# Optimization experiments

Hardware: AMD Instinct MI355X
Metric: run time of the kernel (lower is better)

## Reference

```python
import jax, jax.numpy as jnp
import numpy as np

BN_EPS = 1e-4  # matches torch.nn.BatchNorm1d(eps=0.0001)

def setup_inputs() -> dict:
    key = jax.random.key(0)
    ks = jax.random.split(key, 8)
    N, T, D_in, D_out = 512, 64, 1024, 1024
    return {
        "input_feature_st": jax.random.randint(ks[0], (N, T, D_in), 0, 2).astype(jnp.float32),
        "input_features_sc": jax.random.normal(ks[1], (N, D_in), dtype=jnp.float32),
        "weight": jax.random.normal(ks[2], (D_out, D_in), dtype=jnp.float32) * 0.03,
        "bias": jax.random.normal(ks[3], (D_out,), dtype=jnp.float32) * 0.1,
        "gamma": jax.random.normal(ks[4], (D_out,), dtype=jnp.float32) * 2.0,  # nn.init.normal_(bn.weight, 0, 2.0)
        "beta": jnp.zeros((D_out,), dtype=jnp.float32),
        "running_mean": jax.random.normal(ks[5], (D_out,), dtype=jnp.float32) * 0.1,
        "running_var": jax.random.uniform(ks[6], (D_out,), dtype=jnp.float32, minval=0.5, maxval=1.5),
    }

def _if_scan(pot_in, bias_step):
    # pot_in: (N, T, D_out); bias_step: (D_out,) -> spikes (N, T, D_out)
    pot0 = jnp.zeros(pot_in.shape[::2], dtype=pot_in.dtype)  # (N, D_out)
    def step(pot, p_t):
        pot = pot + p_t + bias_step
        spk = (pot >= 1.0).astype(pot.dtype)
        return pot - spk, spk
    _, spikes_t = jax.lax.scan(step, pot0, jnp.swapaxes(pot_in, 0, 1))  # (T, N, D)
    return jnp.swapaxes(spikes_t, 0, 1)

def reference(input_feature_st, input_features_sc, weight, bias, gamma, beta, running_mean, running_var):
    T = input_feature_st.shape[1]
    # ANN path: Linear + BN (eval stats) + ReLU
    lin = input_features_sc @ weight.T + bias                      # (N, D_out)
    out_bn = gamma * (lin - running_mean) / jnp.sqrt(running_var + BN_EPS) + beta
    ann_output = jax.nn.relu(out_bn)
    # Fold BN into weights for the SNN path (note: no eps, as in source)
    ratio = gamma / jnp.sqrt(running_var)
    w_norm = weight * ratio[:, None]                               # (D_out, D_in)
    b_norm = (bias - running_mean) * ratio + beta                  # (D_out,)
    # Integrate-and-fire scan over T
    pot_in = jnp.einsum("ntd,od->nto", input_feature_st, w_norm)  # (N, T, D_out)
    spike_out = _if_scan(pot_in, b_norm / T)
    spike_count_out = jnp.sum(spike_out, axis=1)                   # (N, D_out)
    return spike_out, spike_count_out
```

## Files before the change

### kernel.cpp

```cpp
#include <hip/hip_runtime.h>
#include <hip/hip_bf16.h>

typedef float  float4v __attribute__((ext_vector_type(4)));
typedef short  short8v __attribute__((ext_vector_type(8)));
typedef short  short4v __attribute__((ext_vector_type(4)));
typedef __bf16 bf16x8  __attribute__((ext_vector_type(8)));
typedef float  f32x4   __attribute__((ext_vector_type(4)));

constexpr int NB = 512, T = 64, DIN = 1024, DOUT = 1024;

constexpr size_t ABF_BYTES = (size_t)NB * T * DIN * 2;
constexpr size_t WN_BYTES  = (size_t)DOUT * DIN * 2;
constexpr size_t WS_BF16   = ABF_BYTES + WN_BYTES;

__device__ __forceinline__ short f2bf_rne(float x) {
    return __builtin_bit_cast(short, __float2bfloat16(x));
}
__device__ __forceinline__ short f2bf_trunc(float x) {
    return (short)(__builtin_bit_cast(unsigned int, x) >> 16);
}
__device__ __forceinline__ void load_lds_16B(const void* g, void* l) {
    __builtin_amdgcn_global_load_lds(
        (const __attribute__((address_space(1))) unsigned int*)g,
        (__attribute__((address_space(3))) unsigned int*)l, 16, 0, 0);
}

constexpr int PREP_A_BLOCKS = NB * T * DIN / 8 / 256;
constexpr int PREP_W_BLOCKS = DOUT * DIN / 4 / 256;

__global__ void __launch_bounds__(256)
prep_fused(const float* __restrict__ A, short* __restrict__ Abf,
           const float* __restrict__ W, const float* __restrict__ gamma,
           const float* __restrict__ rvar, short* __restrict__ Wn) {
    const int b = blockIdx.x;
    if (b < PREP_A_BLOCKS) {
        int idx = b * 256 + threadIdx.x;
        const float4v* p = (const float4v*)A + (size_t)idx * 2;
        float4v v0 = __builtin_nontemporal_load(p);
        float4v v1 = __builtin_nontemporal_load(p + 1);
        short8v s;
        #pragma unroll
        for (int j = 0; j < 4; j++) {
            s[j]     = f2bf_trunc(v0[j]);
            s[j + 4] = f2bf_trunc(v1[j]);
        }
        *((short8v*)Abf + idx) = s;
    } else {
        int idx = (b - PREP_A_BLOCKS) * 256 + threadIdx.x;
        int o = idx >> 8;
        float r = gamma[o] / sqrtf(rvar[o]);
        float4v w = ((const float4v*)W)[idx];
        short4v s;
        #pragma unroll
        for (int j = 0; j < 4; j++) s[j] = f2bf_rne(w[j] * r);
        ((short4v*)Wn)[idx] = s;
    }
}

__global__ void __launch_bounds__(256)
fold_w_kernel(const float* __restrict__ W, const float* __restrict__ gamma,
              const float* __restrict__ rvar, short* __restrict__ Wn) {
    int idx = blockIdx.x * 256 + threadIdx.x;
    int o = idx >> 8;
    float r = gamma[o] / sqrtf(rvar[o]);
    float4v w = ((const float4v*)W)[idx];
    short4v s;
    #pragma unroll
    for (int j = 0; j < 4; j++) s[j] = f2bf_rne(w[j] * r);
    ((short4v*)Wn)[idx] = s;
}

constexpr int BM2 = 256, BN2 = 256, BK2 = 32;
constexpr int NSTEP2 = DIN / BK2;
constexpr int BUFB   = (BM2 + BN2) * BK2 * 2;
constexpr int BREG   = BM2 * BK2 * 2;

__global__ void __launch_bounds__(512, 2)
snn_gemm_if_256(const short* __restrict__ Abf,
                const short* __restrict__ Wn,
                const float* __restrict__ bias, const float* __restrict__ gamma,
                const float* __restrict__ beta, const float* __restrict__ rmean,
                const float* __restrict__ rvar, float* __restrict__ out) {
    __shared__ __align__(16) char sm[3 * BUFB];
    __shared__ float bstepS[BN2];

    const int tid = threadIdx.x;
    const int oB  = blockIdx.x * BN2;
    const int bs  = blockIdx.y;

    if (tid < BN2) {
        int o = oB + tid;
        float r = gamma[o] / sqrtf(rvar[o]);
        bstepS[tid] = ((bias[o] - rmean[o]) * r + beta[o]) * (1.0f / 64.0f);
    }

    const int lane = tid & 63;
    const int wv   = tid >> 6;
    const int wr   = wv >> 2;
    const int wc   = wv & 3;
    const int l15  = lane & 15;
    const int quad = lane >> 4;

    int aOff[8], bOff[4];
    #pragma unroll
    for (int mi = 0; mi < 8; mi++) {
        int r = wr * 128 + mi * 16 + l15;
        aOff[mi] = (r * 4 + (quad ^ ((r >> 1) & 3))) * 16;
    }
    #pragma unroll
    for (int ni = 0; ni < 4; ni++) {
        int r = wc * 64 + ni * 16 + l15;
        bOff[ni] = BREG + (r * 4 + (quad ^ ((r >> 1) & 3))) * 16;
    }

    f32x4 acc[8][4] = {};

    const int s0 = tid, s1 = 512 + tid;
    const int r0 = s0 >> 2, r1 = s1 >> 2;
    const int c0 = (s0 & 3) ^ ((r0 >> 1) & 3);
    const int c1 = (s1 & 3) ^ ((r1 >> 1) & 3);
    const short* gA0 = Abf + (size_t)(bs * BM2 + r0) * DIN + c0 * 8;
    const short* gA1 = Abf + (size_t)(bs * BM2 + r1) * DIN + c1 * 8;
    const short* gB0 = Wn + (size_t)(oB + r0) * DIN + c0 * 8;
    const short* gB1 = Wn + (size_t)(oB + r1) * DIN + c1 * 8;
    const int dA0 = s0 * 16, dA1 = s1 * 16;
    const int dB0 = BREG + s0 * 16, dB1 = BREG + s1 * 16;

    auto STAGE = [&](int bufB) {
        load_lds_16B(gA0, sm + bufB + dA0);
        load_lds_16B(gA1, sm + bufB + dA1);
        load_lds_16B(gB0, sm + bufB + dB0);
        load_lds_16B(gB1, sm + bufB + dB1);
        gA0 += BK2; gA1 += BK2; gB0 += BK2; gB1 += BK2;
    };
    auto COMPUTE = [&](int bufB) {
        const char* base = sm + bufB;
        bf16x8 af[8], bv[4];
        #pragma unroll
        for (int mi = 0; mi < 8; mi++)
            af[mi] = __builtin_bit_cast(bf16x8, *(const short8v*)(base + aOff[mi]));
        #pragma unroll
        for (int ni = 0; ni < 4; ni++)
            bv[ni] = __builtin_bit_cast(bf16x8, *(const short8v*)(base + bOff[ni]));
        __builtin_amdgcn_s_setprio(1);
        #pragma unroll
        for (int mi = 0; mi < 8; mi++)
            #pragma unroll
            for (int ni = 0; ni < 4; ni++)
                acc[mi][ni] = __builtin_amdgcn_mfma_f32_16x16x32_bf16(
                    af[mi], bv[ni], acc[mi][ni], 0, 0, 0);
        __builtin_amdgcn_s_setprio(0);
    };

    STAGE(0);
    STAGE(BUFB);
    asm volatile("s_waitcnt vmcnt(4)" ::: "memory");
    __builtin_amdgcn_sched_barrier(0);
    __builtin_amdgcn_s_barrier();
    __builtin_amdgcn_sched_barrier(0);

    int cb = 0, sb = 2 * BUFB;
    #pragma unroll 1
    for (int t = 0; t < NSTEP2 - 2; ++t) {
        STAGE(sb);
        COMPUTE(cb);
        asm volatile("s_waitcnt vmcnt(4)" ::: "memory");
        __builtin_amdgcn_sched_barrier(0);
        __builtin_amdgcn_s_barrier();
        __builtin_amdgcn_sched_barrier(0);
        cb = (cb == 2 * BUFB) ? 0 : cb + BUFB;
        sb = (sb == 2 * BUFB) ? 0 : sb + BUFB;
    }
    COMPUTE(0);
    asm volatile("s_waitcnt vmcnt(0)" ::: "memory");
    __builtin_amdgcn_sched_barrier(0);
    __builtin_amdgcn_s_barrier();
    __builtin_amdgcn_sched_barrier(0);
    COMPUTE(BUFB);

    __syncthreads();

    float* potS = (float*)sm;
    #pragma unroll
    for (int s = 0; s < 4; ++s) {
        if (wr == (s >> 1)) {
            const int mib = (s & 1) * 4;
            #pragma unroll
            for (int m2 = 0; m2 < 4; ++m2)
                #pragma unroll
                for (int ni = 0; ni < 4; ++ni)
                    #pragma unroll
                    for (int r = 0; r < 4; ++r) {
                        int rl  = m2 * 16 + quad * 4 + r;
                        int col = (wc * 64 + ni * 16 + l15) ^ (quad << 3);
                        potS[rl * BN2 + col] = acc[mib + m2][ni][r];
                    }
        }
        __syncthreads();
        if (tid < BN2) {
            int n = bs * 4 + s;
            float pot = 0.f, cnt = 0.f;
            const float bst = bstepS[tid];
            float* so = out + (size_t)n * T * DOUT + oB + tid;
            for (int t = 0; t < T; t++) {
                pot += potS[t * BN2 + (tid ^ (((t >> 2) & 3) << 3))] + bst;
                float spk = (pot >= 1.0f) ? 1.0f : 0.0f;
                pot -= spk;
                cnt += spk;
                __builtin_nontemporal_store(spk, so + (size_t)t * DOUT);
            }
            __builtin_nontemporal_store(
                cnt, out + (size_t)NB * T * DOUT + (size_t)n * DOUT + oB + tid);
        }
        __syncthreads();
    }
}


constexpr int BM = 128, BN = 128, BK = 64;
constexpr int LDA_F = 72;
constexpr int A_BYTES_F = BM * LDA_F * 2;
constexpr int SMEM_F = A_BYTES_F + BN * BK * 2;

template <bool PREFOLD>
__global__ void __launch_bounds__(256)
snn_gemm_if(const float* __restrict__ A, const float* __restrict__ W,
            const short* __restrict__ Wn,
            const float* __restrict__ bias, const float* __restrict__ gamma,
            const float* __restrict__ beta, const float* __restrict__ rmean,
            const float* __restrict__ rvar, float* __restrict__ out) {
    __shared__ __align__(16) char smem[SMEM_F];
    __shared__ float ratioS[BN];
    __shared__ float bstepS[BN];
    short* AsS  = (short*)smem;
    short* BsS  = (short*)(smem + A_BYTES_F);
    float* potS = (float*)smem;

    const int tid   = threadIdx.x;
    const int by    = blockIdx.y;
    const int oBase = blockIdx.x * BN;

    if (tid < BN) {
        int o = oBase + tid;
        float r = gamma[o] / sqrtf(rvar[o]);
        ratioS[tid] = r;
        bstepS[tid] = ((bias[o] - rmean[o]) * r + beta[o]) * (1.0f / 64.0f);
    }
    __syncthreads();

    const int lane = tid & 63;
    const int wv   = tid >> 6;
    const int wr   = wv & 1;
    const int wc   = wv >> 1;
    const int l15  = lane & 15;
    const int quad = lane >> 4;

    f32x4 acc[4][4] = {};
    const float* Ab = A + (size_t)by * BM * DIN;

    for (int kb = 0; kb < DIN; kb += BK) {
        float4v av[4][2];
        #pragma unroll
        for (int i = 0; i < 4; i++) {
            int g = i * 256 + tid;
            int r = g >> 3, k8 = g & 7;
            const float4v* p = (const float4v*)(Ab + (size_t)r * DIN + kb + k8 * 8);
            av[i][0] = p[0];
            av[i][1] = p[1];
        }
        float4v bv[4][2];
        if constexpr (!PREFOLD) {
            #pragma unroll
            for (int i = 0; i < 4; i++) {
                int slot = i * 256 + tid;
                int r = slot >> 3, k8 = (slot & 7) ^ (r & 7);
                const float4v* p = (const float4v*)(W + (size_t)(oBase + r) * DIN + kb + k8 * 8);
                bv[i][0] = p[0];
                bv[i][1] = p[1];
            }
        }
        __syncthreads();

        if constexpr (PREFOLD) {
            #pragma unroll
            for (int i = 0; i < 4; i++) {
                int slot = i * 256 + tid;
                int r = slot >> 3, k8 = (slot & 7) ^ (r & 7);
                load_lds_16B(Wn + (size_t)(oBase + r) * DIN + kb + k8 * 8,
                             BsS + (size_t)slot * 8);
            }
        } else {
            #pragma unroll
            for (int i = 0; i < 4; i++) {
                int slot = i * 256 + tid;
                int r = slot >> 3;
                float rt = ratioS[r];
                short8v s;
                #pragma unroll
                for (int j = 0; j < 4; j++) {
                    s[j]     = f2bf_rne(bv[i][0][j] * rt);
                    s[j + 4] = f2bf_rne(bv[i][1][j] * rt);
                }
                *(short8v*)(BsS + (size_t)slot * 8) = s;
            }
        }
        #pragma unroll
        for (int i = 0; i < 4; i++) {
            int g = i * 256 + tid;
            int r = g >> 3, k8 = g & 7;
            short8v s;
            #pragma unroll
            for (int j = 0; j < 4; j++) {
                s[j]     = f2bf_trunc(av[i][0][j]);
                s[j + 4] = f2bf_trunc(av[i][1][j]);
            }
            *(short8v*)(&AsS[r * LDA_F + k8 * 8]) = s;
        }
        __syncthreads();

        #pragma unroll
        for (int ks = 0; ks < 2; ks++) {
            bf16x8 af[4], bfv[4];
            #pragma unroll
            for (int mi = 0; mi < 4; mi++)
                af[mi] = __builtin_bit_cast(bf16x8,
                    *(const short8v*)(&AsS[(wr * 64 + mi * 16 + l15) * LDA_F + ks * 32 + quad * 8]));
            #pragma unroll
            for (int ni = 0; ni < 4; ni++) {
                int row  = wc * 64 + ni * 16 + l15;
                int slot = row * 8 + ((ks * 4 + quad) ^ (l15 & 7));
                bfv[ni] = __builtin_bit_cast(bf16x8, *(const short8v*)(BsS + (size_t)slot * 8));
            }
            #pragma unroll
            for (int mi = 0; mi < 4; mi++)
                #pragma unroll
                for (int ni = 0; ni < 4; ni++)
                    acc[mi][ni] = __builtin_amdgcn_mfma_f32_16x16x32_bf16(
                        af[mi], bfv[ni], acc[mi][ni], 0, 0, 0);
        }
    }

    __syncthreads();

    #pragma unroll 1
    for (int s = 0; s < 2; s++) {
        if (wr == s) {
            #pragma unroll
            for (int mi = 0; mi < 4; mi++)
                #pragma unroll
                for (int ni = 0; ni < 4; ni++)
                    #pragma unroll
                    for (int r = 0; r < 4; r++)
                        potS[(mi * 16 + quad * 4 + r) * BN + wc * 64 + ni * 16 + l15] =
                            acc[mi][ni][r];
        }
        __syncthreads();
        if (tid < BN) {
            int n = by * 2 + s;
            float pot = 0.f, cnt = 0.f;
            const float bst = bstepS[tid];
            float* so = out + (size_t)n * T * DOUT + oBase + tid;
            for (int t = 0; t < T; t++) {
                pot += potS[t * BN + tid] + bst;
                float spk = (pot >= 1.0f) ? 1.0f : 0.0f;
                pot -= spk;
                cnt += spk;
                so[(size_t)t * DOUT] = spk;
            }
            out[(size_t)NB * T * DOUT + (size_t)n * DOUT + oBase + tid] = cnt;
        }
        __syncthreads();
    }
}

extern "C" void kernel_launch(void* const* d_in, const int* in_sizes, int n_in,
                              void* d_out, int out_size, void* d_ws, size_t ws_size,
                              hipStream_t stream) {
    const float* A     = (const float*)d_in[0];
    const float* W     = (const float*)d_in[2];
    const float* bias  = (const float*)d_in[3];
    const float* gamma = (const float*)d_in[4];
    const float* beta  = (const float*)d_in[5];
    const float* rmean = (const float*)d_in[6];
    const float* rvar  = (const float*)d_in[7];
    float* out = (float*)d_out;

    if (d_ws != nullptr && ws_size >= WS_BF16) {
        short* Abf = (short*)d_ws;
        short* Wn  = (short*)((char*)d_ws + ABF_BYTES);
        prep_fused<<<PREP_A_BLOCKS + PREP_W_BLOCKS, 256, 0, stream>>>(
            A, Abf, W, gamma, rvar, Wn);
        dim3 grid(DOUT / BN2, NB / 4);
        snn_gemm_if_256<<<grid, 512, 0, stream>>>(Abf, Wn, bias, gamma, beta,
                                                  rmean, rvar, out);
    } else if (d_ws != nullptr && ws_size >= WN_BYTES) {
        short* Wn = (short*)d_ws;
        fold_w_kernel<<<DOUT * DIN / 4 / 256, 256, 0, stream>>>(W, gamma, rvar, Wn);
        dim3 grid(DOUT / BN, NB / 2);
        snn_gemm_if<true><<<grid, 256, 0, stream>>>(A, W, Wn, bias, gamma, beta,
                                                    rmean, rvar, out);
    } else {
        dim3 grid(DOUT / BN, NB / 2);
        snn_gemm_if<false><<<grid, 256, 0, stream>>>(A, W, nullptr, bias, gamma, beta,
                                                     rmean, rvar, out);
    }
}
```

Baseline: 320.7 us.

## Restructure 256x256 SNN GEMM into 9-slot LDS ring with interleaved quarter-tile MFMA phases

The bf16 GEMM main loop now uses BK=64 and a 9-slot LDS ring in 16KB half-tile slots. Loads for future A/B halves are issued between four MFMA phases, each bracketed by barriers, so global-to-LDS traffic overlaps compute at a finer grain. The grid becomes 1D with an XCD-aware remap of block index to work tile for better L2 locality. The IF scan epilogue now uses all 512 threads, two samples at a time, instead of 256. LDS use rises to about 144KB, which could limit occupancy to one block per CU despite the launch bound of 2, and the extra barriers add sync cost.

After: 321.4 us. About the same (+0.2%).

```diff
diff --git a/kernel.cpp b/kernel.cpp
--- a/kernel.cpp
+++ b/kernel.cpp
@@ -70,10 +70,11 @@
     ((short4v*)Wn)[idx] = s;
 }
 
-constexpr int BM2 = 256, BN2 = 256, BK2 = 32;
-constexpr int NSTEP2 = DIN / BK2;
-constexpr int BUFB   = (BM2 + BN2) * BK2 * 2;
-constexpr int BREG   = BM2 * BK2 * 2;
+constexpr int BM2 = 256, BN2 = 256, BK2 = 64;
+constexpr int NT2   = DIN / BK2;
+constexpr int SLOT  = 16384;
+constexpr int NSLOT = 9;
+constexpr int RINGB = NSLOT * SLOT;
 
 __global__ void __launch_bounds__(512, 2)
 snn_gemm_if_256(const short* __restrict__ Abf,
@@ -81,18 +82,21 @@
                 const float* __restrict__ bias, const float* __restrict__ gamma,
                 const float* __restrict__ beta, const float* __restrict__ rmean,
                 const float* __restrict__ rvar, float* __restrict__ out) {
-    __shared__ __align__(16) char sm[3 * BUFB];
+    __shared__ __align__(16) char sm[RINGB];
     __shared__ float bstepS[BN2];
 
     const int tid = threadIdx.x;
-    const int oB  = blockIdx.x * BN2;
-    const int bs  = blockIdx.y;
+    const int work = (blockIdx.x & 7) * 64 + (blockIdx.x >> 3);
+    const int oB = (work & 3) * BN2;
+    const int rg = work >> 2;
 
     if (tid < BN2) {
         int o = oB + tid;
         float r = gamma[o] / sqrtf(rvar[o]);
         bstepS[tid] = ((bias[o] - rmean[o]) * r + beta[o]) * (1.0f / 64.0f);
     }
+    asm volatile("s_waitcnt vmcnt(0)" ::: "memory");
+    __builtin_amdgcn_sched_barrier(0);
 
     const int lane = tid & 63;
     const int wv   = tid >> 6;
@@ -101,116 +105,172 @@
     const int l15  = lane & 15;
     const int quad = lane >> 4;
 
-    int aOff[8], bOff[4];
-    #pragma unroll
-    for (int mi = 0; mi < 8; mi++) {
-        int r = wr * 128 + mi * 16 + l15;
-        aOff[mi] = (r * 4 + (quad ^ ((r >> 1) & 3))) * 16;
-    }
-    #pragma unroll
-    for (int ni = 0; ni < 4; ni++) {
-        int r = wc * 64 + ni * 16 + l15;
-        bOff[ni] = BREG + (r * 4 + (quad ^ ((r >> 1) & 3))) * 16;
-    }
+    const int D0 = l15 * 128 + ((quad ^ (l15 & 7)) * 16);
+    const int D1 = l15 * 128 + (((4 + quad) ^ (l15 & 7)) * 16);
+    const int bWoff = (wc & 1) * 8192;
+
+    const int row0 = tid >> 3,         ck0 = (tid & 7) ^ (row0 & 7);
+    const int row1 = (512 + tid) >> 3, ck1 = ((512 + tid) & 7) ^ (row1 & 7);
+    const short* gA0a = Abf + (size_t)(rg * BM2 + row0) * DIN + ck0 * 8;
+    const short* gA0b = Abf + (size_t)(rg * BM2 + row1) * DIN + ck1 * 8;
+    const short* gA1a = gA0a + (size_t)128 * DIN;
+    const short* gA1b = gA0b + (size_t)128 * DIN;
+    const short* gB0a = Wn + (size_t)(oB + row0) * DIN + ck0 * 8;
+    const short* gB0b = Wn + (size_t)(oB + row1) * DIN + ck1 * 8;
+    const short* gB1a = gB0a + (size_t)128 * DIN;
+    const short* gB1b = gB0b + (size_t)128 * DIN;
+
+    auto STAGE = [&](const short*& g0, const short*& g1, int dstB) {
+        load_lds_16B(g0, sm + dstB + tid * 16);
+        load_lds_16B(g1, sm + dstB + 8192 + tid * 16);
+        g0 += BK2; g1 += BK2;
+    };
+    auto LD8 = [&](const char* p) {
+        return __builtin_bit_cast(bf16x8, *(const short8v*)p);
+    };
 
     f32x4 acc[8][4] = {};
 
-    const int s0 = tid, s1 = 512 + tid;
-    const int r0 = s0 >> 2, r1 = s1 >> 2;
-    const int c0 = (s0 & 3) ^ ((r0 >> 1) & 3);
-    const int c1 = (s1 & 3) ^ ((r1 >> 1) & 3);
-    const short* gA0 = Abf + (size_t)(bs * BM2 + r0) * DIN + c0 * 8;
-    const short* gA1 = Abf + (size_t)(bs * BM2 + r1) * DIN + c1 * 8;
-    const short* gB0 = Wn + (size_t)(oB + r0) * DIN + c0 * 8;
-    const short* gB1 = Wn + (size_t)(oB + r1) * DIN + c1 * 8;
-    const int dA0 = s0 * 16, dA1 = s1 * 16;
-    const int dB0 = BREG + s0 * 16, dB1 = BREG + s1 * 16;
-
-    auto STAGE = [&](int bufB) {
-        load_lds_16B(gA0, sm + bufB + dA0);
-        load_lds_16B(gA1, sm + bufB + dA1);
-        load_lds_16B(gB0, sm + bufB + dB0);
-        load_lds_16B(gB1, sm + bufB + dB1);
-        gA0 += BK2; gA1 += BK2; gB0 += BK2; gB1 += BK2;
-    };
-    auto COMPUTE = [&](int bufB) {
-        const char* base = sm + bufB;
-        bf16x8 af[8], bv[4];
-        #pragma unroll
-        for (int mi = 0; mi < 8; mi++)
-            af[mi] = __builtin_bit_cast(bf16x8, *(const short8v*)(base + aOff[mi]));
-        #pragma unroll
-        for (int ni = 0; ni < 4; ni++)
-            bv[ni] = __builtin_bit_cast(bf16x8, *(const short8v*)(base + bOff[ni]));
-        __builtin_amdgcn_s_setprio(1);
-        #pragma unroll
-        for (int mi = 0; mi < 8; mi++)
-            #pragma unroll
-            for (int ni = 0; ni < 4; ni++)
-                acc[mi][ni] = __builtin_amdgcn_mfma_f32_16x16x32_bf16(
-                    af[mi], bv[ni], acc[mi][ni], 0, 0, 0);
-        __builtin_amdgcn_s_setprio(0);
-    };
-
-    STAGE(0);
-    STAGE(BUFB);
-    asm volatile("s_waitcnt vmcnt(4)" ::: "memory");
+    int rbA0 = 0, rbA1 = SLOT, rbB0 = 2 * SLOT, rbB1 = 3 * SLOT;
+    int wb0 = 5 * SLOT, wb1 = 6 * SLOT, wb2 = 7 * SLOT, wb3 = 8 * SLOT;
+    auto adv = [](int& x) { x += 4 * SLOT; if (x >= RINGB) x -= RINGB; };
+
+    STAGE(gA0a, gA0b, 0);
+    STAGE(gA1a, gA1b, SLOT);
+    STAGE(gB0a, gB0b, 2 * SLOT);
+    STAGE(gB1a, gB1b, 3 * SLOT);
+    STAGE(gA0a, gA0b, 4 * SLOT);
+    asm volatile("s_waitcnt vmcnt(2)" ::: "memory");
     __builtin_amdgcn_sched_barrier(0);
     __builtin_amdgcn_s_barrier();
     __builtin_amdgcn_sched_barrier(0);
 
-    int cb = 0, sb = 2 * BUFB;
     #pragma unroll 1
-    for (int t = 0; t < NSTEP2 - 2; ++t) {
-        STAGE(sb);
-        COMPUTE(cb);
-        asm volatile("s_waitcnt vmcnt(4)" ::: "memory");
+    for (int t = 0; t < NT2; ++t) {
+        const char* pA = sm + (wr ? rbA1 : rbA0);
+        const char* pB = sm + ((wc & 2) ? rbB1 : rbB0) + bWoff;
+        bf16x8 af[4][2], bfv[2][2], bf2[2][2];
+
+        if (t < NT2 - 1) { STAGE(gA1a, gA1b, wb0); STAGE(gB0a, gB0b, wb1); }
+        #pragma unroll
+        for (int mi = 0; mi < 4; mi++) {
+            af[mi][0] = LD8(pA + mi * 2048 + D0);
+            af[mi][1] = LD8(pA + mi * 2048 + D1);
+        }
+        #pragma unroll
+        for (int ni = 0; ni < 2; ni++) {
+            bfv[ni][0] = LD8(pB + ni * 2048 + D0);
+            bfv[ni][1] = LD8(pB + ni * 2048 + D1);
+        }
+        __builtin_amdgcn_s_barrier();
+        __builtin_amdgcn_s_setprio(1);
+        #pragma unroll
+        for (int mi = 0; mi < 4; mi++)
+            #pragma unroll
+            for (int ni = 0; ni < 2; ni++)
+                #pragma unroll
+                for (int ks = 0; ks < 2; ks++)
+                    acc[mi][ni] = __builtin_amdgcn_mfma_f32_16x16x32_bf16(
+                        af[mi][ks], bfv[ni][ks], acc[mi][ni], 0, 0, 0);
+        __builtin_amdgcn_s_setprio(0);
+        __builtin_amdgcn_s_barrier();
+
+        if (t < NT2 - 1) STAGE(gB1a, gB1b, wb2);
+        if (t < NT2 - 2) STAGE(gA0a, gA0b, wb3);
+        #pragma unroll
+        for (int ni = 0; ni < 2; ni++) {
+            bf2[ni][0] = LD8(pB + (2 + ni) * 2048 + D0);
+            bf2[ni][1] = LD8(pB + (2 + ni) * 2048 + D1);
+        }
+        __builtin_amdgcn_s_barrier();
+        __builtin_amdgcn_s_setprio(1);
+        #pragma unroll
+        for (int mi = 0; mi < 4; mi++)
+            #pragma unroll
+            for (int ni = 0; ni < 2; ni++)
+                #pragma unroll
+                for (int ks = 0; ks < 2; ks++)
+                    acc[mi][2 + ni] = __builtin_amdgcn_mfma_f32_16x16x32_bf16(
+                        af[mi][ks], bf2[ni][ks], acc[mi][2 + ni], 0, 0, 0);
+        __builtin_amdgcn_s_setprio(0);
+        __builtin_amdgcn_s_barrier();
+
+        #pragma unroll
+        for (int mi = 0; mi < 4; mi++) {
+            af[mi][0] = LD8(pA + (4 + mi) * 2048 + D0);
+            af[mi][1] = LD8(pA + (4 + mi) * 2048 + D1);
+        }
+        __builtin_amdgcn_s_barrier();
+        __builtin_amdgcn_s_setprio(1);
+        #pragma unroll
+        for (int mi = 0; mi < 4; mi++)
+            #pragma unroll
+            for (int ni = 0; ni < 2; ni++)
+                #pragma unroll
+                for (int ks = 0; ks < 2; ks++)
+                    acc[4 + mi][ni] = __builtin_amdgcn_mfma_f32_16x16x32_bf16(
+                        af[mi][ks], bfv[ni][ks], acc[4 + mi][ni], 0, 0, 0);
+        __builtin_amdgcn_s_setprio(0);
+        __builtin_amdgcn_s_barrier();
+
+        __builtin_amdgcn_s_setprio(1);
+        #pragma unroll
+        for (int mi = 0; mi < 4; mi++)
+            #pragma unroll
+            for (int ni = 0; ni < 2; ni++)
+                #pragma unroll
+                for (int ks = 0; ks < 2; ks++)
+                    acc[4 + mi][2 + ni] = __builtin_amdgcn_mfma_f32_16x16x32_bf16(
+                        af[mi][ks], bf2[ni][ks], acc[4 + mi][2 + ni], 0, 0, 0);
+        __builtin_amdgcn_s_setprio(0);
+
+        if (t == NT2 - 2) {
+            asm volatile("s_waitcnt vmcnt(0)" ::: "memory");
+        } else {
+            asm volatile("s_waitcnt vmcnt(2)" ::: "memory");
+        }
         __builtin_amdgcn_sched_barrier(0);
         __builtin_amdgcn_s_barrier();
         __builtin_amdgcn_sched_barrier(0);
-        cb = (cb == 2 * BUFB) ? 0 : cb + BUFB;
-        sb = (sb == 2 * BUFB) ? 0 : sb + BUFB;
-    }
-    COMPUTE(0);
-    asm volatile("s_waitcnt vmcnt(0)" ::: "memory");
-    __builtin_amdgcn_sched_barrier(0);
-    __builtin_amdgcn_s_barrier();
-    __builtin_amdgcn_sched_barrier(0);
-    COMPUTE(BUFB);
+
+        adv(rbA0); adv(rbA1); adv(rbB0); adv(rbB1);
+        adv(wb0);  adv(wb1);  adv(wb2);  adv(wb3);
+    }
 
     __syncthreads();
 
     float* potS = (float*)sm;
-    #pragma unroll
-    for (int s = 0; s < 4; ++s) {
-        if (wr == (s >> 1)) {
-            const int mib = (s & 1) * 4;
-            #pragma unroll
-            for (int m2 = 0; m2 < 4; ++m2)
-                #pragma unroll
-                for (int ni = 0; ni < 4; ++ni)
+    #pragma unroll 1
+    for (int rd = 0; rd < 2; ++rd) {
+        if (wr == rd) {
+            #pragma unroll
+            for (int mi = 0; mi < 8; mi++)
+                #pragma unroll
+                for (int ni = 0; ni < 4; ni++)
                     #pragma unroll
-                    for (int r = 0; r < 4; ++r) {
-                        int rl  = m2 * 16 + quad * 4 + r;
-                        int col = (wc * 64 + ni * 16 + l15) ^ (quad << 3);
-                        potS[rl * BN2 + col] = acc[mib + m2][ni][r];
+                    for (int r = 0; r < 4; r++) {
+                        int rowl = mi * 16 + quad * 4 + r;
+                        int col  = (wc * 64 + ni * 16 + l15) ^ (quad << 3);
+                        potS[rowl * BN2 + col] = acc[mi][ni][r];
                     }
         }
         __syncthreads();
-        if (tid < BN2) {
-            int n = bs * 4 + s;
+        {
+            int sl = tid >> 8;
+            int c  = tid & 255;
+            int n  = rg * 4 + rd * 2 + sl;
             float pot = 0.f, cnt = 0.f;
-            const float bst = bstepS[tid];
-            float* so = out + (size_t)n * T * DOUT + oB + tid;
-            for (int t = 0; t < T; t++) {
-                pot += potS[t * BN2 + (tid ^ (((t >> 2) & 3) << 3))] + bst;
+            const float bst = bstepS[c];
+            float* so = out + (size_t)n * T * DOUT + oB + c;
+            for (int tt = 0; tt < T; tt++) {
+                pot += potS[(sl * 64 + tt) * BN2 + (c ^ (((tt >> 2) & 3) << 3))] + bst;
                 float spk = (pot >= 1.0f) ? 1.0f : 0.0f;
                 pot -= spk;
                 cnt += spk;
-                __builtin_nontemporal_store(spk, so + (size_t)t * DOUT);
+                __builtin_nontemporal_store(spk, so + (size_t)tt * DOUT);
             }
             __builtin_nontemporal_store(
-                cnt, out + (size_t)NB * T * DOUT + (size_t)n * DOUT + oB + tid);
+                cnt, out + (size_t)NB * T * DOUT + (size_t)n * DOUT + oB + c);
         }
         __syncthreads();
     }
@@ -390,9 +450,8 @@
         short* Wn  = (short*)((char*)d_ws + ABF_BYTES);
         prep_fused<<<PREP_A_BLOCKS + PREP_W_BLOCKS, 256, 0, stream>>>(
             A, Abf, W, gamma, rvar, Wn);
-        dim3 grid(DOUT / BN2, NB / 4);
-        snn_gemm_if_256<<<grid, 512, 0, stream>>>(Abf, Wn, bias, gamma, beta,
-                                                  rmean, rvar, out);
+        snn_gemm_if_256<<<dim3(512), 512, 0, stream>>>(Abf, Wn, bias, gamma, beta,
+                                                       rmean, rvar, out);
     } else if (d_ws != nullptr && ws_size >= WN_BYTES) {
         short* Wn = (short*)d_ws;
         fold_w_kernel<<<DOUT * DIN / 4 / 256, 256, 0, stream>>>(W, gamma, rvar, Wn);
```

## Use 1024-thread blocks with smaller per-wave tiles and all-thread IF scan

Applied to the files above, without the earlier changes.

Doubles the block to 1024 threads (16 waves), so each wave now owns a 64x64 accumulator tile instead of 128x64. This cuts register pressure and lets all threads take part in the integrate-and-fire epilogue: four samples are scanned in parallel, in chunks of 16 timesteps. It also flattens the grid into a 1D launch with a swizzled block-to-tile mapping meant to improve L2 reuse. The trade-off is fewer MFMAs per LDS fragment load, which lowers operand reuse per wave, and launch_bounds(1024,4) may be unattainable given the LDS size.

Result: slower. 346.1 us (+7.9%).

```diff
diff --git a/kernel.cpp b/kernel.cpp
--- a/kernel.cpp
+++ b/kernel.cpp
@@ -71,11 +71,11 @@
 }
 
 constexpr int BM2 = 256, BN2 = 256, BK2 = 32;
-constexpr int NSTEP2 = DIN / BK2;
-constexpr int BUFB   = (BM2 + BN2) * BK2 * 2;
-constexpr int BREG   = BM2 * BK2 * 2;
-
-__global__ void __launch_bounds__(512, 2)
+constexpr int NT2  = DIN / BK2;
+constexpr int BUFB = (BM2 + BN2) * BK2 * 2;
+constexpr int BREG = BM2 * BK2 * 2;
+
+__global__ void __launch_bounds__(1024, 4)
 snn_gemm_if_256(const short* __restrict__ Abf,
                 const short* __restrict__ Wn,
                 const float* __restrict__ bias, const float* __restrict__ gamma,
@@ -85,14 +85,17 @@
     __shared__ float bstepS[BN2];
 
     const int tid = threadIdx.x;
-    const int oB  = blockIdx.x * BN2;
-    const int bs  = blockIdx.y;
+    const int work = (blockIdx.x & 7) * 64 + (blockIdx.x >> 3);
+    const int oB = (work & 3) * BN2;
+    const int rg = work >> 2;
 
     if (tid < BN2) {
         int o = oB + tid;
         float r = gamma[o] / sqrtf(rvar[o]);
         bstepS[tid] = ((bias[o] - rmean[o]) * r + beta[o]) * (1.0f / 64.0f);
     }
+    asm volatile("s_waitcnt vmcnt(0)" ::: "memory");
+    __builtin_amdgcn_sched_barrier(0);
 
     const int lane = tid & 63;
     const int wv   = tid >> 6;
@@ -101,119 +104,105 @@
     const int l15  = lane & 15;
     const int quad = lane >> 4;
 
-    int aOff[8], bOff[4];
+    int aOff[4], bOff[4];
     #pragma unroll
-    for (int mi = 0; mi < 8; mi++) {
-        int r = wr * 128 + mi * 16 + l15;
-        aOff[mi] = (r * 4 + (quad ^ ((r >> 1) & 3))) * 16;
-    }
-    #pragma unroll
-    for (int ni = 0; ni < 4; ni++) {
-        int r = wc * 64 + ni * 16 + l15;
-        bOff[ni] = BREG + (r * 4 + (quad ^ ((r >> 1) & 3))) * 16;
-    }
-
-    f32x4 acc[8][4] = {};
-
-    const int s0 = tid, s1 = 512 + tid;
-    const int r0 = s0 >> 2, r1 = s1 >> 2;
-    const int c0 = (s0 & 3) ^ ((r0 >> 1) & 3);
-    const int c1 = (s1 & 3) ^ ((r1 >> 1) & 3);
-    const short* gA0 = Abf + (size_t)(bs * BM2 + r0) * DIN + c0 * 8;
-    const short* gA1 = Abf + (size_t)(bs * BM2 + r1) * DIN + c1 * 8;
-    const short* gB0 = Wn + (size_t)(oB + r0) * DIN + c0 * 8;
-    const short* gB1 = Wn + (size_t)(oB + r1) * DIN + c1 * 8;
-    const int dA0 = s0 * 16, dA1 = s1 * 16;
-    const int dB0 = BREG + s0 * 16, dB1 = BREG + s1 * 16;
+    for (int i = 0; i < 4; i++) {
+        int ra = wr * 64 + i * 16 + l15;
+        int rb = wc * 64 + i * 16 + l15;
+        aOff[i] = ra * 64 + ((quad ^ ((ra >> 1) & 3)) * 16);
+        bOff[i] = BREG + rb * 64 + ((quad ^ ((rb >> 1) & 3)) * 16);
+    }
+
+    const int srow = tid >> 2;
+    const int gck  = (tid & 3) ^ ((srow >> 1) & 3);
+    const short* gA = Abf + (size_t)(rg * BM2 + srow) * DIN + gck * 8;
+    const short* gB = Wn + (size_t)(oB + srow) * DIN + gck * 8;
+    const int dA = tid * 16;
+    const int dB = BREG + tid * 16;
 
     auto STAGE = [&](int bufB) {
-        load_lds_16B(gA0, sm + bufB + dA0);
-        load_lds_16B(gA1, sm + bufB + dA1);
-        load_lds_16B(gB0, sm + bufB + dB0);
-        load_lds_16B(gB1, sm + bufB + dB1);
-        gA0 += BK2; gA1 += BK2; gB0 += BK2; gB1 += BK2;
+        load_lds_16B(gA, sm + bufB + dA);
+        load_lds_16B(gB, sm + bufB + dB);
+        gA += BK2; gB += BK2;
     };
-    auto COMPUTE = [&](int bufB) {
-        const char* base = sm + bufB;
-        bf16x8 af[8], bv[4];
-        #pragma unroll
-        for (int mi = 0; mi < 8; mi++)
-            af[mi] = __builtin_bit_cast(bf16x8, *(const short8v*)(base + aOff[mi]));
-        #pragma unroll
-        for (int ni = 0; ni < 4; ni++)
-            bv[ni] = __builtin_bit_cast(bf16x8, *(const short8v*)(base + bOff[ni]));
+    auto LD8 = [&](const char* p) {
+        return __builtin_bit_cast(bf16x8, *(const short8v*)p);
+    };
+
+    f32x4 acc[4][4] = {};
+
+    STAGE(0);
+    STAGE(BUFB);
+    asm volatile("s_waitcnt vmcnt(2)" ::: "memory");
+    __builtin_amdgcn_sched_barrier(0);
+    __builtin_amdgcn_s_barrier();
+    __builtin_amdgcn_sched_barrier(0);
+
+    int cb = 0, sb = 2 * BUFB;
+    #pragma unroll 1
+    for (int t = 0; t < NT2; ++t) {
+        if (t < NT2 - 2) STAGE(sb);
+        const char* base = sm + cb;
+        bf16x8 af[4], bv[4];
+        #pragma unroll
+        for (int i = 0; i < 4; i++) af[i] = LD8(base + aOff[i]);
+        #pragma unroll
+        for (int i = 0; i < 4; i++) bv[i] = LD8(base + bOff[i]);
         __builtin_amdgcn_s_setprio(1);
         #pragma unroll
-        for (int mi = 0; mi < 8; mi++)
+        for (int mi = 0; mi < 4; mi++)
             #pragma unroll
             for (int ni = 0; ni < 4; ni++)
                 acc[mi][ni] = __builtin_amdgcn_mfma_f32_16x16x32_bf16(
                     af[mi], bv[ni], acc[mi][ni], 0, 0, 0);
         __builtin_amdgcn_s_setprio(0);
-    };
-
-    STAGE(0);
-    STAGE(BUFB);
-    asm volatile("s_waitcnt vmcnt(4)" ::: "memory");
-    __builtin_amdgcn_sched_barrier(0);
-    __builtin_amdgcn_s_barrier();
-    __builtin_amdgcn_sched_barrier(0);
-
-    int cb = 0, sb = 2 * BUFB;
-    #pragma unroll 1
-    for (int t = 0; t < NSTEP2 - 2; ++t) {
-        STAGE(sb);
-        COMPUTE(cb);
-        asm volatile("s_waitcnt vmcnt(4)" ::: "memory");
+
+        if (t < NT2 - 2) {
+            asm volatile("s_waitcnt vmcnt(2)" ::: "memory");
+        } else {
+            asm volatile("s_waitcnt vmcnt(0)" ::: "memory");
+        }
         __builtin_amdgcn_sched_barrier(0);
         __builtin_amdgcn_s_barrier();
         __builtin_amdgcn_sched_barrier(0);
+
         cb = (cb == 2 * BUFB) ? 0 : cb + BUFB;
         sb = (sb == 2 * BUFB) ? 0 : sb + BUFB;
     }
-    COMPUTE(0);
-    asm volatile("s_waitcnt vmcnt(0)" ::: "memory");
-    __builtin_amdgcn_sched_barrier(0);
-    __builtin_amdgcn_s_barrier();
-    __builtin_amdgcn_sched_barrier(0);
-    COMPUTE(BUFB);
-
-    __syncthreads();
 
     float* potS = (float*)sm;
-    #pragma unroll
-    for (int s = 0; s < 4; ++s) {
-        if (wr == (s >> 1)) {
-            const int mib = (s & 1) * 4;
-            #pragma unroll
-            for (int m2 = 0; m2 < 4; ++m2)
-                #pragma unroll
-                for (int ni = 0; ni < 4; ++ni)
-                    #pragma unroll
-                    for (int r = 0; r < 4; ++r) {
-                        int rl  = m2 * 16 + quad * 4 + r;
-                        int col = (wc * 64 + ni * 16 + l15) ^ (quad << 3);
-                        potS[rl * BN2 + col] = acc[mib + m2][ni][r];
-                    }
-        }
-        __syncthreads();
-        if (tid < BN2) {
-            int n = bs * 4 + s;
-            float pot = 0.f, cnt = 0.f;
-            const float bst = bstepS[tid];
-            float* so = out + (size_t)n * T * DOUT + oB + tid;
-            for (int t = 0; t < T; t++) {
-                pot += potS[t * BN2 + (tid ^ (((t >> 2) & 3) << 3))] + bst;
-                float spk = (pot >= 1.0f) ? 1.0f : 0.0f;
-                pot -= spk;
-                cnt += spk;
-                __builtin_nontemporal_store(spk, so + (size_t)t * DOUT);
-            }
-            __builtin_nontemporal_store(
-                cnt, out + (size_t)NB * T * DOUT + (size_t)n * DOUT + oB + tid);
-        }
-        __syncthreads();
-    }
+    float pot = 0.f, cnt = 0.f;
+    const int sc_s = tid >> 8;
+    const int sc_c = tid & 255;
+    const float bst = bstepS[sc_c];
+    float* so = out + (size_t)(rg * 4 + sc_s) * T * DOUT + oB + sc_c;
+
+    #pragma unroll 1
+    for (int j = 0; j < 4; ++j) {
+        #pragma unroll
+        for (int ni = 0; ni < 4; ni++)
+            #pragma unroll
+            for (int r = 0; r < 4; r++) {
+                int i   = quad * 4 + r;
+                int col = (wc * 64 + ni * 16 + l15) ^ (quad << 3);
+                potS[wr * 4096 + i * 256 + col] = acc[j][ni][r];
+            }
+        __syncthreads();
+        #pragma unroll
+        for (int i = 0; i < 16; i++) {
+            int t = j * 16 + i;
+            pot += potS[sc_s * 4096 + i * 256 +
+                        (sc_c ^ (((i >> 2) & 3) << 3))] + bst;
+            float spk = (pot >= 1.0f) ? 1.0f : 0.0f;
+            pot -= spk;
+            cnt += spk;
+            __builtin_nontemporal_store(spk, so + (size_t)t * DOUT);
+        }
+        __syncthreads();
+    }
+    __builtin_nontemporal_store(
+        cnt, out + (size_t)NB * T * DOUT +
+             (size_t)(rg * 4 + sc_s) * DOUT + oB + sc_c);
 }
 
 
@@ -390,9 +379,8 @@
         short* Wn  = (short*)((char*)d_ws + ABF_BYTES);
         prep_fused<<<PREP_A_BLOCKS + PREP_W_BLOCKS, 256, 0, stream>>>(
             A, Abf, W, gamma, rvar, Wn);
-        dim3 grid(DOUT / BN2, NB / 4);
-        snn_gemm_if_256<<<grid, 512, 0, stream>>>(Abf, Wn, bias, gamma, beta,
-                                                  rmean, rvar, out);
+        snn_gemm_if_256<<<dim3(512), 1024, 0, stream>>>(Abf, Wn, bias, gamma, beta,
+                                                        rmean, rvar, out);
     } else if (d_ws != nullptr && ws_size >= WN_BYTES) {
         short* Wn = (short*)d_ws;
         fold_w_kernel<<<DOUT * DIN / 4 / 256, 256, 0, stream>>>(W, gamma, rvar, Wn);
```
